# Kernel tuning notes

Hardware: AMD Instinct MI355X
Metric: run time of the kernel (lower is better)

The kernel has to match this reference:

```python
import jax, jax.numpy as jnp
import numpy as np

B, T, N = 16, 2048, 24
K, C_IN, C0, C1 = 3, 1, 64, 64
KS, PRED_LEN = 3, 24
EPS = 1e-5


def _norm_laplacian(adj):
    # L = D^-1/2 A^T D^-1/2 (matches scipy path: (A D^-1/2)^T D^-1/2)
    d = adj.sum(axis=1)
    dis = jnp.where(d > 0, 1.0 / jnp.sqrt(d), 0.0)
    return dis[:, None] * adj.T * dis[None, :]


def _cheb_stack(L, k_terms):
    polys = [jnp.eye(N, dtype=L.dtype), L]
    for _ in range(2, k_terms):
        polys.append(2.0 * L @ polys[-1] - polys[-2])
    return jnp.stack(polys[:k_terms])  # (K, N, N)


def _causal_conv(x, w, b, dilation):
    ks = w.shape[-1]
    pad = (ks - 1) * dilation
    x = jnp.pad(x, ((0, 0), (0, 0), (0, 0), (pad, 0)))
    y = jax.lax.conv_general_dilated(
        x, w, window_strides=(1, 1), padding='VALID',
        rhs_dilation=(1, dilation),
        dimension_numbers=('NCHW', 'OIHW', 'NCHW'))
    return y + b[None, :, None, None]


def _bn(x, g, be):
    # training-mode batch norm over (B, N, T) per channel
    mu = x.mean(axis=(0, 2, 3), keepdims=True)
    var = x.var(axis=(0, 2, 3), keepdims=True)
    return g[None, :, None, None] * (x - mu) * jax.lax.rsqrt(var + EPS) + be[None, :, None, None]


def setup_inputs() -> dict:
    key = jax.random.key(0)
    ks = jax.random.split(key, 16)
    s = 0.05
    return {
        'batch_x': jax.random.normal(ks[0], (B, T, N), jnp.float32),
        'adj': jax.random.uniform(ks[1], (N, N), jnp.float32),
        'theta': jax.random.normal(ks[2], (K, C_IN, C0), jnp.float32),  # Theta per Cheb term
        'w1a': jax.random.normal(ks[3], (C0, C0, 1, KS), jnp.float32) * s,
        'b1a': jnp.zeros((C0,), jnp.float32),
        'g1a': jnp.ones((C0,), jnp.float32), 'be1a': jnp.zeros((C0,), jnp.float32),
        'w1b': jax.random.normal(ks[4], (C0, C0, 1, KS), jnp.float32) * s,
        'b1b': jnp.zeros((C0,), jnp.float32),
        'g1b': jnp.ones((C0,), jnp.float32), 'be1b': jnp.zeros((C0,), jnp.float32),
        'w2a': jax.random.normal(ks[5], (C1, C0, 1, KS), jnp.float32) * s,
        'b2a': jnp.zeros((C1,), jnp.float32),
        'g2a': jnp.ones((C1,), jnp.float32), 'be2a': jnp.zeros((C1,), jnp.float32),
        'w2b': jax.random.normal(ks[6], (C1, C1, 1, KS), jnp.float32) * s,
        'b2b': jnp.zeros((C1,), jnp.float32),
        'g2b': jnp.ones((C1,), jnp.float32), 'be2b': jnp.zeros((C1,), jnp.float32),
        'w_end': jax.random.normal(ks[7], (C1 // 2, C1, 1, 1), jnp.float32) * s,
        'b_end': jnp.zeros((C1 // 2,), jnp.float32),
        'w_end1': jax.random.normal(ks[8], (1, C1 // 2, 1, 2), jnp.float32) * s,
        'b_end1': jnp.zeros((1,), jnp.float32),
    }


def reference(batch_x, adj, theta,
              w1a, b1a, g1a, be1a, w1b, b1b, g1b, be1b,
              w2a, b2a, g2a, be2a, w2b, b2b, g2b, be2b,
              w_end, b_end, w_end1, b_end1):
    # (B, T, N) -> (B, 1, N, T)
    x = jnp.transpose(batch_x, (0, 2, 1))[:, None, :, :]

    # --- Cheb_conv: fused over K terms and all timesteps ---
    L = _norm_laplacian(adj)
    Tk = _cheb_stack(L, K)                       # (K, N, N)
    xp = jnp.transpose(x, (0, 2, 1, 3))          # (B, N, C_in, T)
    # out[b,o,n,t] = sum_{k,m,c} xp[b,m,c,t] Tk[k,m,n] theta[k,c,o]
    gc = jnp.einsum('bmct,kmn,kco->bont', xp, Tk, theta)  # (B, C0, N, T)

    # --- TCN block 1 (dilation 1), residual is identity (C0 == C0) ---
    h = jax.nn.relu(_bn(_causal_conv(gc, w1a, b1a, 1), g1a, be1a))
    h = jax.nn.relu(_bn(_causal_conv(h, w1b, b1b, 1), g1b, be1b))
    out0 = jax.nn.relu(h + gc)

    # --- TCN block 2 (dilation 2), residual identity (C0 == C1), no final relu ---
    h = jax.nn.relu(_bn(_causal_conv(out0, w2a, b2a, 2), g2a, be2a))
    h = jax.nn.relu(_bn(_causal_conv(h, w2b, b2b, 2), g2b, be2b))
    out = h + out0                               # (B, C1, N, T)

    # --- head: 1x1 conv + relu, then (1,2) valid conv -> 1 channel ---
    e = jax.lax.conv_general_dilated(out, w_end, (1, 1), 'VALID',
                                     dimension_numbers=('NCHW', 'OIHW', 'NCHW'))
    e = jax.nn.relu(e + b_end[None, :, None, None])
    e = jax.lax.conv_general_dilated(e, w_end1, (1, 1), 'VALID',
                                     dimension_numbers=('NCHW', 'OIHW', 'NCHW'))
    e = e + b_end1[None, :, None, None]          # (B, 1, N, T-1)
    e = e[:, 0, :, -PRED_LEN:]                   # (B, N, pred_len)
    return jnp.transpose(e, (0, 2, 1))           # (B, pred_len, N)
```

## Files before the change

kernel.cpp:

```cpp
#include <hip/hip_runtime.h>
#include <cmath>

#define TPB 256

typedef __attribute__((ext_vector_type(8)))  short short8;
typedef __attribute__((ext_vector_type(16))) float float16;

static constexpr int  BB   = 16;
static constexpr int  TDIM = 2048;
static constexpr int  NN   = 24;
static constexpr int  P    = BB * NN;
static constexpr int  C    = 64;
static constexpr int  TILE = 256;
static constexpr int  NBT  = TDIM / TILE;
static constexpr int  NSHARD = 64;
static constexpr float INV_CNT = 1.0f / 786432.0f;

static constexpr size_t OFF_TK    = 0;
static constexpr size_t OFF_WEFF  = 6912;
static constexpr size_t OFF_WFRAG = 9216;
static constexpr size_t OFF_ST    = 82944;
static constexpr size_t OFF_BNAB  = 214016;
static constexpr size_t OFF_O0    = 216320;
static constexpr size_t OFF_YT    = 2673920;
static constexpr size_t OFF_S     = 5131520;
static constexpr size_t OFF_YA    = 14568704;
static constexpr size_t OFF_YB    = 115232000;

__device__ __forceinline__ unsigned short f2bf(float f) {
    unsigned int i = __float_as_uint(f);
    i += 0x7FFFu + ((i >> 16) & 1u);
    return (unsigned short)(i >> 16);
}
__device__ __forceinline__ float bf2f(unsigned short u) {
    return __uint_as_float((unsigned)u << 16);
}
__device__ __forceinline__ unsigned pk2bf(float a, float b) {
    unsigned ua = __float_as_uint(a) + 0x8000u;
    unsigned ub = __float_as_uint(b) + 0x8000u;
    return __builtin_amdgcn_perm(ub, ua, 0x07060302u);
}
__device__ __forceinline__ int xidx(int tt, int ci) {
    return tt * 64 + (((ci ^ (tt & 7)) << 3));
}

__global__ __launch_bounds__(TPB)
void prep_kernel(const float* __restrict__ adj, const float* __restrict__ theta,
                 const float* __restrict__ w1a,
                 const float* __restrict__ w1b, const float* __restrict__ w2a,
                 const float* __restrict__ w2b,
                 float* __restrict__ tk, float* __restrict__ weff,
                 unsigned short* __restrict__ wf, float* __restrict__ stats)
{
    const int tid = threadIdx.x;
    if (blockIdx.x < 144) {
        int e = blockIdx.x * TPB + tid;
        int conv = e / 12288, r = e % 12288;
        int oh = r / 6144; r %= 6144;
        int kc = r / 512;  r %= 512;
        int lane = r / 8;
        int jj = r % 8;
        int o = oh * 32 + (lane & 31);
        int K = kc * 16 + (lane >> 5) * 8 + jj;
        int j = K / 64, c2 = K % 64;
        const float* w = (conv == 0) ? w1b : ((conv == 1) ? w2a : w2b);
        wf[e] = f2bf(w[(o * 64 + c2) * 3 + j]);
        return;
    }

    __shared__ float disl[24];
    __shared__ float Ll[576];
    __shared__ float T2l[576];

    for (int e = tid; e < 4 * 8192; e += TPB) stats[e] = 0.f;

    if (tid < 24) {
        float d = 0.f;
        for (int j = 0; j < 24; ++j) d += adj[tid * 24 + j];
        disl[tid] = (d > 0.f) ? 1.0f / sqrtf(d) : 0.f;
    }
    __syncthreads();
    for (int e = tid; e < 576; e += TPB) {
        int i = e / 24, j = e % 24;
        Ll[e] = disl[i] * adj[j * 24 + i] * disl[j];
    }
    __syncthreads();
    for (int e = tid; e < 576; e += TPB) {
        int i = e / 24, j = e % 24;
        float a = 0.f;
        for (int m = 0; m < 24; ++m) a += Ll[i * 24 + m] * Ll[m * 24 + j];
        T2l[e] = 2.f * a - ((i == j) ? 1.f : 0.f);
    }
    __syncthreads();
    for (int e = tid; e < 576; e += TPB) {
        int i = e / 24, j = e % 24;
        tk[e]        = (i == j) ? 1.f : 0.f;
        tk[576 + e]  = Ll[e];
        tk[1152 + e] = T2l[e];
    }
    for (int e = tid; e < 576; e += TPB) {
        int o = e / 9, k = (e % 9) / 3, j = e % 3;
        float a = 0.f;
        for (int c2 = 0; c2 < 64; ++c2)
            a += w1a[(o * 64 + c2) * 3 + j] * theta[k * 64 + c2];
        weff[(k * 3 + j) * 64 + o] = a;
    }
}

__global__ __launch_bounds__(TPB)
void bnprep_kernel(const float* __restrict__ stats, const float* __restrict__ g,
                   const float* __restrict__ be, float2* __restrict__ ab)
{
    const int tid = threadIdx.x;
    const int ch = tid >> 2, q = tid & 3;
    float s1 = 0.f, s2 = 0.f;
    #pragma unroll
    for (int u = 0; u < 16; ++u) {
        int sh = q * 16 + u;
        s1 += stats[ch * 64 + sh];
        s2 += stats[(64 + ch) * 64 + sh];
    }
    s1 += __shfl_xor(s1, 1); s1 += __shfl_xor(s1, 2);
    s2 += __shfl_xor(s2, 1); s2 += __shfl_xor(s2, 2);
    if (q == 0) {
        float mu  = s1 * INV_CNT;
        float var = s2 * INV_CNT - mu * mu;
        float a = g[ch] * (1.0f / sqrtf(var + 1e-5f));
        ab[ch] = make_float2(a, be[ch] - mu * a);
    }
}

__global__ __launch_bounds__(TPB)
void s_kernel(const float* __restrict__ bx, const float* __restrict__ tk,
              float* __restrict__ sbuf)
{
    __shared__ float bxs[256 * 25];
    __shared__ float tkl[576];
    const int tid = threadIdx.x;
    const int blk = blockIdx.x;
    const int b  = blk / 24;
    const int r  = blk % 24;
    const int k  = r >> 3;
    const int t0 = (r & 7) * 256;

    for (int e = tid; e < 576; e += TPB) tkl[e] = tk[k * 576 + e];
    for (int e = tid; e < 256 * 24; e += TPB) {
        int t = e / 24, m = e % 24;
        bxs[t * 25 + m] = bx[((long)b * TDIM + t0 + t) * NN + m];
    }
    __syncthreads();

    const int t = tid;
    float acc[24];
    #pragma unroll
    for (int n = 0; n < 24; ++n) acc[n] = 0.f;
    for (int m = 0; m < 24; ++m) {
        float xb = bxs[t * 25 + m];
        const float* tr = tkl + m * 24;
        #pragma unroll
        for (int n = 0; n < 24; ++n) acc[n] = fmaf(xb, tr[n], acc[n]);
    }
    for (int n = 0; n < 24; ++n)
        sbuf[((long)k * P + b * NN + n) * TDIM + t0 + t] = acc[n];
}

__global__ __launch_bounds__(TPB)
void stats1a_kernel(const float* __restrict__ sbuf, const float* __restrict__ weff,
                    float* __restrict__ statsOut)
{
    __shared__ float4 ssl4[3 * 66];
    __shared__ float4 wl4[144];
    __shared__ float  part[4][2][64];
    const int tid = threadIdx.x;
    const int blk = blockIdx.x;
    const int p  = blk >> 3;
    const int t0 = (blk & 7) * 256;

    for (int e = tid; e < 576; e += TPB) ((float*)wl4)[e] = weff[e];
    for (int e = tid; e < 3 * 65; e += TPB) {
        int k = e / 65, u4 = e % 65;
        int t = t0 - 4 + u4 * 4;
        float4 v = make_float4(0.f, 0.f, 0.f, 0.f);
        if (t >= 0) v = *(const float4*)(sbuf + ((long)k * P + p) * TDIM + t);
        ssl4[k * 66 + u4] = v;
    }
    __syncthreads();

    const int oq = tid & 7;
    const int tq = tid >> 3;
    float acc[8][8];
    #pragma unroll
    for (int i = 0; i < 8; ++i)
        #pragma unroll
        for (int ti = 0; ti < 8; ++ti) acc[i][ti] = 0.f;

    #pragma unroll
    for (int k = 0; k < 3; ++k) {
        float4 x0 = ssl4[k * 66 + tq * 2];
        float4 x1 = ssl4[k * 66 + tq * 2 + 1];
        float4 x2 = ssl4[k * 66 + tq * 2 + 2];
        float xv[12] = { x0.x,x0.y,x0.z,x0.w, x1.x,x1.y,x1.z,x1.w, x2.x,x2.y,x2.z,x2.w };
        #pragma unroll
        for (int j = 0; j < 3; ++j) {
            float4 w0 = wl4[(k * 3 + j) * 16 + oq * 2];
            float4 w1 = wl4[(k * 3 + j) * 16 + oq * 2 + 1];
            float wv[8] = { w0.x,w0.y,w0.z,w0.w, w1.x,w1.y,w1.z,w1.w };
            #pragma unroll
            for (int i = 0; i < 8; ++i)
                #pragma unroll
                for (int ti = 0; ti < 8; ++ti)
                    acc[i][ti] = fmaf(wv[i], xv[ti + 2 + j], acc[i][ti]);
        }
    }

    float s1v[8], s2v[8];
    #pragma unroll
    for (int i = 0; i < 8; ++i) {
        float a1 = 0.f, a2 = 0.f;
        #pragma unroll
        for (int ti = 0; ti < 8; ++ti) { a1 += acc[i][ti]; a2 += acc[i][ti] * acc[i][ti]; }
        s1v[i] = a1; s2v[i] = a2;
    }
    #pragma unroll
    for (int m = 8; m < 64; m <<= 1) {
        #pragma unroll
        for (int i = 0; i < 8; ++i) {
            s1v[i] += __shfl_xor(s1v[i], m);
            s2v[i] += __shfl_xor(s2v[i], m);
        }
    }
    const int wave = tid >> 6, lane = tid & 63;
    if (lane < 8) {
        #pragma unroll
        for (int i = 0; i < 8; ++i) {
            part[wave][0][oq * 8 + i] = s1v[i];
            part[wave][1][oq * 8 + i] = s2v[i];
        }
    }
    __syncthreads();
    if (tid < 128) {
        int s = tid >> 6, o = tid & 63;
        float tot = part[0][s][o] + part[1][s][o] + part[2][s][o] + part[3][s][o];
        atomicAdd(&statsOut[(s * 64 + o) * NSHARD + (blk & 63)], tot);
    }
}

template<int MODE>
__global__ __launch_bounds__(TPB, 4)
void conv_mfma(const float* __restrict__ sbuf, const unsigned short* __restrict__ yin,
               unsigned short* __restrict__ yout, float* __restrict__ ytail,
               const unsigned short* __restrict__ wf, const float* __restrict__ weff,
               const float2* __restrict__ bnab, float* __restrict__ statsOut,
               const float* __restrict__ theta, float* __restrict__ o0s)
{
    constexpr int SCR = (MODE == 0) ? (792 + 576) : ((MODE == 1) ? (792 + 192) : 512);
    __shared__ unsigned short Xl[260 * 64];
    __shared__ float  scratch[SCR];
    __shared__ float2 abl[64];

    float* const ssl   = scratch;
    float* const weffl = scratch + 792;
    float* const thl   = scratch + 792;
    float* const parts = scratch;

    const int tid  = threadIdx.x;
    const int lane = tid & 63;
    const int w    = tid >> 6;
    const int oh   = w & 1;
    const int l31  = lane & 31;
    const int h    = lane >> 5;
    const int blk  = blockIdx.x;
    const int p    = blk >> 3;
    const int tile = blk & 7;
    const int t0   = tile * TILE;

    short8 af[12];
    #pragma unroll
    for (int kc = 0; kc < 12; ++kc)
        af[kc] = *((const short8*)wf + (oh * 12 + kc) * 64 + lane);

    if (tid < 64) abl[tid] = bnab[tid];
    if (MODE == 0)
        for (int e = tid; e < 576; e += TPB) weffl[e] = weff[e];
    if (MODE == 1)
        if (tid < 192) thl[tid] = theta[tid];
    if (MODE <= 1) {
        for (int e = tid; e < 3 * 66; e += TPB) {
            int k = e / 66, u4 = e % 66;
            int t = t0 - 8 + u4 * 4;
            float4 v = make_float4(0.f, 0.f, 0.f, 0.f);
            if (t >= 0) v = *(const float4*)(sbuf + ((long)k * P + p) * TDIM + t);
            *(float4*)(ssl + k * 264 + u4 * 4) = v;
        }
    }
    __syncthreads();

    const unsigned short* yinb = (MODE >= 1)
        ? (yin + ((long)p * TDIM + t0 - 4) * 64) : nullptr;
    for (int e = tid; e < 260 * 8; e += TPB) {
        const int tt = e >> 3, cb = e & 7;
        const int t = t0 - 4 + tt;
        float xv[8];
        if (t < 0) {
            #pragma unroll
            for (int r = 0; r < 8; ++r) xv[r] = 0.f;
        } else if (MODE == 0) {
            float sv[9];
            #pragma unroll
            for (int k = 0; k < 3; ++k)
                #pragma unroll
                for (int j = 0; j < 3; ++j)
                    sv[k * 3 + j] = ssl[k * 264 + tt + 2 + j];
            #pragma unroll
            for (int r = 0; r < 8; ++r) {
                int c = cb * 8 + r;
                float raw = 0.f;
                #pragma unroll
                for (int u = 0; u < 9; ++u)
                    raw = fmaf(weffl[u * 64 + c], sv[u], raw);
                float2 ab = abl[c];
                xv[r] = fmaxf(fmaf(ab.x, raw, ab.y), 0.f);
            }
        } else {
            short8 yv8 = *(const short8*)(yinb + (long)e * 8);
            float gcb[3];
            if (MODE == 1) {
                gcb[0] = ssl[      tt + 4];
                gcb[1] = ssl[264 + tt + 4];
                gcb[2] = ssl[528 + tt + 4];
            }
            #pragma unroll
            for (int r = 0; r < 8; ++r) {
                int c = cb * 8 + r;
                float2 ab = abl[c];
                float v = bf2f((unsigned short)yv8[r]);
                float hh = fmaxf(fmaf(ab.x, v, ab.y), 0.f);
                if (MODE == 1) {
                    float gc = thl[c] * gcb[0] + thl[64 + c] * gcb[1] + thl[128 + c] * gcb[2];
                    hh = fmaxf(hh + gc, 0.f);
                }
                xv[r] = hh;
            }
        }
        if (MODE == 1 && tile == 7 && tt >= 235) {
            #pragma unroll
            for (int r = 0; r < 8; ++r)
                o0s[(long)p * 1600 + (cb * 8 + r) * 25 + (tt - 235)] = xv[r];
        }
        uint4 pk;
        pk.x = pk2bf(xv[0], xv[1]);
        pk.y = pk2bf(xv[2], xv[3]);
        pk.z = pk2bf(xv[4], xv[5]);
        pk.w = pk2bf(xv[6], xv[7]);
        *(uint4*)(Xl + xidx(tt, cb)) = pk;
    }
    __syncthreads();

    float16 acc[4];
    #pragma unroll
    for (int i = 0; i < 4; ++i)
        #pragma unroll
        for (int r = 0; r < 16; ++r) acc[i][r] = 0.f;

    const int tqb = (w >> 1) * 4;
    #pragma unroll
    for (int kc = 0; kc < 12; ++kc) {
        const int j = kc >> 2;
        const int roff = (MODE == 0) ? (2 + j) : (2 * j);
        const int ci = (kc & 3) * 2 + h;
        #pragma unroll
        for (int i = 0; i < 4; ++i) {
            int row = (tqb + i) * 32 + l31 + roff;
            short8 bfr = *(const short8*)(Xl + xidx(row, ci));
            acc[i] = __builtin_amdgcn_mfma_f32_32x32x16_bf16(af[kc], bfr, acc[i], 0, 0, 0);
        }
    }

    if (MODE <= 1) {
        __syncthreads();

        #pragma unroll
        for (int i = 0; i < 4; ++i) {
            int tl = (tqb + i) * 32 + l31;
            #pragma unroll
            for (int qq = 0; qq < 4; ++qq) {
                int ci = oh * 4 + qq;
                uint2 pk;
                pk.x = pk2bf(acc[i][4 * qq + 0], acc[i][4 * qq + 1]);
                pk.y = pk2bf(acc[i][4 * qq + 2], acc[i][4 * qq + 3]);
                *(uint2*)(Xl + xidx(tl, ci) + 4 * h) = pk;
            }
        }
        __syncthreads();

        const int cb = tid & 7;
        unsigned short* youtb = yout + ((long)p * TDIM + t0) * 64;
        float s1[8], s2[8];
        #pragma unroll
        for (int r = 0; r < 8; ++r) { s1[r] = 0.f; s2[r] = 0.f; }
        for (int e = tid; e < 2048; e += TPB) {
            int tt = e >> 3;
            uint4 v = *(const uint4*)(Xl + xidx(tt, cb));
            *(uint4*)(youtb + (long)e * 8) = v;
            unsigned uu[4] = { v.x, v.y, v.z, v.w };
            #pragma unroll
            for (int qq = 0; qq < 4; ++qq) {
                float f0 = __uint_as_float(uu[qq] << 16);
                float f1 = __uint_as_float(uu[qq] & 0xFFFF0000u);
                s1[2 * qq]     += f0;  s2[2 * qq]     = fmaf(f0, f0, s2[2 * qq]);
                s1[2 * qq + 1] += f1;  s2[2 * qq + 1] = fmaf(f1, f1, s2[2 * qq + 1]);
            }
        }
        #pragma unroll
        for (int m = 8; m <= 32; m <<= 1) {
            #pragma unroll
            for (int r = 0; r < 8; ++r) {
                s1[r] += __shfl_xor(s1[r], m);
                s2[r] += __shfl_xor(s2[r], m);
            }
        }
        if (lane < 8) {
            float* pw = parts + (w * 8 + lane) * 16;
            #pragma unroll
            for (int r = 0; r < 8; ++r) { pw[r * 2] = s1[r]; pw[r * 2 + 1] = s2[r]; }
        }
        __syncthreads();
        if (tid < 64) {
            int o = tid, cbo = o >> 3, r = o & 7;
            float t1 = 0.f, t2 = 0.f;
            #pragma unroll
            for (int ww = 0; ww < 4; ++ww) {
                t1 += parts[(ww * 8 + cbo) * 16 + r * 2];
                t2 += parts[(ww * 8 + cbo) * 16 + r * 2 + 1];
            }
            atomicAdd(&statsOut[o * NSHARD + (blk & 63)], t1);
            atomicAdd(&statsOut[(64 + o) * NSHARD + (blk & 63)], t2);
        }
    } else {
        if (tile == 7) {
            #pragma unroll
            for (int i = 0; i < 4; ++i) {
                int tg = t0 + (tqb + i) * 32 + l31;
                if (tg >= TDIM - 25) {
                    #pragma unroll
                    for (int r = 0; r < 16; ++r) {
                        int o = oh * 32 + (r & 3) + 8 * (r >> 2) + 4 * h;
                        ytail[((long)p * C + o) * 25 + (tg - (TDIM - 25))] = acc[i][r];
                    }
                }
            }
        }
        float s1[16], s2[16];
        #pragma unroll
        for (int r = 0; r < 16; ++r) {
            float a1 = 0.f, a2 = 0.f;
            #pragma unroll
            for (int i = 0; i < 4; ++i) { float v = acc[i][r]; a1 += v; a2 = fmaf(v, v, a2); }
            s1[r] = a1; s2[r] = a2;
        }
        #pragma unroll
        for (int m = 1; m <= 16; m <<= 1) {
            #pragma unroll
            for (int r = 0; r < 16; ++r) {
                s1[r] += __shfl_xor(s1[r], m);
                s2[r] += __shfl_xor(s2[r], m);
            }
        }
        if (l31 == 0) {
            float* pw = parts + (w * 2 + h) * 32;
            #pragma unroll
            for (int r = 0; r < 16; ++r) { pw[r * 2] = s1[r]; pw[r * 2 + 1] = s2[r]; }
        }
        __syncthreads();
        if (tid < 64) {
            int o = tid;
            int ohh = o >> 5, v = o & 31;
            int hh = (v >> 2) & 1, r = (v & 3) + 4 * (v >> 3);
            float t1 = parts[(ohh * 2 + hh) * 32 + r * 2]
                     + parts[((ohh + 2) * 2 + hh) * 32 + r * 2];
            float t2 = parts[(ohh * 2 + hh) * 32 + r * 2 + 1]
                     + parts[((ohh + 2) * 2 + hh) * 32 + r * 2 + 1];
            atomicAdd(&statsOut[o * NSHARD + (blk & 63)], t1);
            atomicAdd(&statsOut[(64 + o) * NSHARD + (blk & 63)], t2);
        }
    }
}

__global__ __launch_bounds__(TPB)
void end_kernel(const float* __restrict__ ytail, const float* __restrict__ o0s,
                const float2* __restrict__ bnab, const float* __restrict__ w_end,
                const float* __restrict__ b_end, const float* __restrict__ w_end1,
                const float* __restrict__ b_end1, float* __restrict__ out)
{
    __shared__ float2 abl[64];
    __shared__ float outl[64 * 25];
    __shared__ float e1l[32 * 25];
    __shared__ float wendl[2048];
    const int tid = threadIdx.x;
    const int p = blockIdx.x;
    const int b = p / 24, n = p % 24;

    if (tid < 64) abl[tid] = bnab[tid];
    for (int e = tid; e < 2048; e += TPB) wendl[e] = w_end[e];
    __syncthreads();

    for (int e = tid; e < 1600; e += TPB) {
        int c = e / 25, tau = e % 25;
        float v = ytail[((long)p * C + c) * 25 + tau];
        float2 ab = abl[c];
        outl[e] = fmaxf(ab.x * v + ab.y, 0.f) + o0s[(long)p * 1600 + e];
    }
    __syncthreads();
    for (int e = tid; e < 800; e += TPB) {
        int q = e / 25, tau = e % 25;
        float a = b_end[q];
        for (int c = 0; c < 64; ++c)
            a = fmaf(wendl[q * 64 + c], outl[c * 25 + tau], a);
        e1l[e] = fmaxf(a, 0.f);
    }
    __syncthreads();
    if (tid < 24) {
        float a = b_end1[0];
        #pragma unroll
        for (int q = 0; q < 32; ++q)
            a += w_end1[q * 2] * e1l[q * 25 + tid] + w_end1[q * 2 + 1] * e1l[q * 25 + tid + 1];
        out[((long)b * 24 + tid) * 24 + n] = a;
    }
}

extern "C" void kernel_launch(void* const* d_in, const int* in_sizes, int n_in,
                              void* d_out, int out_size, void* d_ws, size_t ws_size,
                              hipStream_t stream)
{
    (void)in_sizes; (void)n_in; (void)out_size; (void)ws_size;
    const float* bx    = (const float*)d_in[0];
    const float* adj   = (const float*)d_in[1];
    const float* theta = (const float*)d_in[2];
    const float* w1a   = (const float*)d_in[3];
    const float* g1a   = (const float*)d_in[5];
    const float* be1a  = (const float*)d_in[6];
    const float* w1b   = (const float*)d_in[7];
    const float* g1b   = (const float*)d_in[9];
    const float* be1b  = (const float*)d_in[10];
    const float* w2a   = (const float*)d_in[11];
    const float* g2a   = (const float*)d_in[13];
    const float* be2a  = (const float*)d_in[14];
    const float* w2b   = (const float*)d_in[15];
    const float* g2b   = (const float*)d_in[17];
    const float* be2b  = (const float*)d_in[18];
    const float* wend  = (const float*)d_in[19];
    const float* bend  = (const float*)d_in[20];
    const float* wend1 = (const float*)d_in[21];
    const float* bend1 = (const float*)d_in[22];

    char* ws = (char*)d_ws;
    float*          tk    = (float*)(ws + OFF_TK);
    float*          weff  = (float*)(ws + OFF_WEFF);
    unsigned short* wf    = (unsigned short*)(ws + OFF_WFRAG);
    float*          stats = (float*)(ws + OFF_ST);
    float2*         bnab  = (float2*)(ws + OFF_BNAB);
    float*          o0s   = (float*)(ws + OFF_O0);
    float*          ytail = (float*)(ws + OFF_YT);
    float*          sb    = (float*)(ws + OFF_S);
    unsigned short* yA    = (unsigned short*)(ws + OFF_YA);
    unsigned short* yB    = (unsigned short*)(ws + OFF_YB);

    prep_kernel   <<<145, TPB, 0, stream>>>(adj, theta, w1a, w1b, w2a, w2b,
                                            tk, weff, wf, stats);
    s_kernel      <<<384, TPB, 0, stream>>>(bx, tk, sb);
    stats1a_kernel<<<P * NBT, TPB, 0, stream>>>(sb, weff, stats);
    bnprep_kernel <<<1, TPB, 0, stream>>>(stats,         g1a, be1a, bnab);

    conv_mfma<0><<<P * NBT, TPB, 0, stream>>>(
        sb, nullptr, yA, nullptr, wf, weff,
        bnab, stats + 8192, nullptr, nullptr);
    bnprep_kernel <<<1, TPB, 0, stream>>>(stats + 8192,  g1b, be1b, bnab + 64);

    conv_mfma<1><<<P * NBT, TPB, 0, stream>>>(
        sb, yA, yB, nullptr, wf + 12288, nullptr,
        bnab + 64, stats + 16384, theta, o0s);
    bnprep_kernel <<<1, TPB, 0, stream>>>(stats + 16384, g2a, be2a, bnab + 128);

    conv_mfma<2><<<P * NBT, TPB, 0, stream>>>(
        sb, yB, nullptr, ytail, wf + 24576, nullptr,
        bnab + 128, stats + 24576, nullptr, nullptr);
    bnprep_kernel <<<1, TPB, 0, stream>>>(stats + 24576, g2b, be2b, bnab + 192);

    end_kernel<<<P, TPB, 0, stream>>>(ytail, o0s, bnab + 192,
                                      wend, bend, wend1, bend1, (float*)d_out);
}
```

Measured before the change: 334.3 us.

## Fuse prep with graph conv, compute BN stats from MFMA accumulators, fold final BN prep

Merges the prep and Chebyshev graph-conv kernels into one launch. Each graph-conv block recomputes the Laplacian and its square locally, and the identity term becomes a plain copy. The output-writing conv modes now take their BN statistics directly from the fp32 MFMA accumulators rather than re-reading the bf16 tile from LDS. The last bnprep launch is folded into end_kernel, and per-thread BN scale/shift and theta values are hoisted into registers. This removes several launches and some LDS work, at the cost of redundant Laplacian work per block. Statistics are now taken before bf16 rounding, which slightly changes the numerics.

```diff
diff --git a/kernel.cpp b/kernel.cpp
--- a/kernel.cpp
+++ b/kernel.cpp
@@ -16,7 +16,6 @@
 static constexpr int  NSHARD = 64;
 static constexpr float INV_CNT = 1.0f / 786432.0f;
 
-static constexpr size_t OFF_TK    = 0;
 static constexpr size_t OFF_WEFF  = 6912;
 static constexpr size_t OFF_WFRAG = 9216;
 static constexpr size_t OFF_ST    = 82944;
@@ -44,17 +43,46 @@
     return tt * 64 + (((ci ^ (tt & 7)) << 3));
 }
 
+__device__ __forceinline__
+void bn_from_stats(const float* __restrict__ statsIn, const float* __restrict__ g,
+                   const float* __restrict__ be, float2* abl, int tid)
+{
+    const int ch = tid >> 2, q = tid & 3;
+    float s1 = 0.f, s2 = 0.f;
+    #pragma unroll
+    for (int u = 0; u < 4; ++u) {
+        float4 a = *(const float4*)(statsIn + tid * 16 + u * 4);
+        float4 b = *(const float4*)(statsIn + 4096 + tid * 16 + u * 4);
+        s1 += a.x + a.y + a.z + a.w;
+        s2 += b.x + b.y + b.z + b.w;
+    }
+    s1 += __shfl_xor(s1, 1); s1 += __shfl_xor(s1, 2);
+    s2 += __shfl_xor(s2, 1); s2 += __shfl_xor(s2, 2);
+    if (q == 0) {
+        float mu  = s1 * INV_CNT;
+        float var = s2 * INV_CNT - mu * mu;
+        float a = g[ch] * (1.0f / sqrtf(var + 1e-5f));
+        abl[ch] = make_float2(a, be[ch] - mu * a);
+    }
+}
+
 __global__ __launch_bounds__(TPB)
-void prep_kernel(const float* __restrict__ adj, const float* __restrict__ theta,
-                 const float* __restrict__ w1a,
-                 const float* __restrict__ w1b, const float* __restrict__ w2a,
-                 const float* __restrict__ w2b,
-                 float* __restrict__ tk, float* __restrict__ weff,
-                 unsigned short* __restrict__ wf, float* __restrict__ stats)
-{
+void prep_s_kernel(const float* __restrict__ adj, const float* __restrict__ theta,
+                   const float* __restrict__ w1a,
+                   const float* __restrict__ w1b, const float* __restrict__ w2a,
+                   const float* __restrict__ w2b, const float* __restrict__ bx,
+                   float* __restrict__ weff, unsigned short* __restrict__ wf,
+                   float* __restrict__ stats, float* __restrict__ sbuf)
+{
+    __shared__ float bxs[256 * 25];
+    __shared__ float disl[24];
+    __shared__ float Ll[576];
+    __shared__ float tkl[576];
     const int tid = threadIdx.x;
-    if (blockIdx.x < 144) {
-        int e = blockIdx.x * TPB + tid;
+    const int blk = blockIdx.x;
+
+    if (blk < 144) {
+        int e = blk * TPB + tid;
         int conv = e / 12288, r = e % 12288;
         int oh = r / 6144; r %= 6144;
         int kc = r / 512;  r %= 512;
@@ -67,44 +95,71 @@
         wf[e] = f2bf(w[(o * 64 + c2) * 3 + j]);
         return;
     }
-
-    __shared__ float disl[24];
-    __shared__ float Ll[576];
-    __shared__ float T2l[576];
-
-    for (int e = tid; e < 4 * 8192; e += TPB) stats[e] = 0.f;
+    if (blk == 144) {
+        for (int e = tid; e < 4 * 8192; e += TPB) stats[e] = 0.f;
+        for (int e = tid; e < 576; e += TPB) {
+            int o = e / 9, k = (e % 9) / 3, j = e % 3;
+            float a = 0.f;
+            for (int c2 = 0; c2 < 64; ++c2)
+                a += w1a[(o * 64 + c2) * 3 + j] * theta[k * 64 + c2];
+            weff[(k * 3 + j) * 64 + o] = a;
+        }
+        return;
+    }
+
+    const int sblk = blk - 145;
+    const int b  = sblk / 24;
+    const int rr = sblk % 24;
+    const int k  = rr >> 3;
+    const int t0 = (rr & 7) * 256;
 
     if (tid < 24) {
         float d = 0.f;
         for (int j = 0; j < 24; ++j) d += adj[tid * 24 + j];
         disl[tid] = (d > 0.f) ? 1.0f / sqrtf(d) : 0.f;
     }
+    for (int e = tid; e < 256 * 24; e += TPB) {
+        int t = e / 24, m = e % 24;
+        bxs[t * 25 + m] = bx[((long)b * TDIM + t0 + t) * NN + m];
+    }
     __syncthreads();
     for (int e = tid; e < 576; e += TPB) {
         int i = e / 24, j = e % 24;
         Ll[e] = disl[i] * adj[j * 24 + i] * disl[j];
     }
     __syncthreads();
-    for (int e = tid; e < 576; e += TPB) {
-        int i = e / 24, j = e % 24;
-        float a = 0.f;
-        for (int m = 0; m < 24; ++m) a += Ll[i * 24 + m] * Ll[m * 24 + j];
-        T2l[e] = 2.f * a - ((i == j) ? 1.f : 0.f);
-    }
-    __syncthreads();
-    for (int e = tid; e < 576; e += TPB) {
-        int i = e / 24, j = e % 24;
-        tk[e]        = (i == j) ? 1.f : 0.f;
-        tk[576 + e]  = Ll[e];
-        tk[1152 + e] = T2l[e];
-    }
-    for (int e = tid; e < 576; e += TPB) {
-        int o = e / 9, k = (e % 9) / 3, j = e % 3;
-        float a = 0.f;
-        for (int c2 = 0; c2 < 64; ++c2)
-            a += w1a[(o * 64 + c2) * 3 + j] * theta[k * 64 + c2];
-        weff[(k * 3 + j) * 64 + o] = a;
-    }
+    if (k == 2) {
+        for (int e = tid; e < 576; e += TPB) {
+            int i = e / 24, j = e % 24;
+            float a = 0.f;
+            for (int m = 0; m < 24; ++m) a += Ll[i * 24 + m] * Ll[m * 24 + j];
+            tkl[e] = 2.f * a - ((i == j) ? 1.f : 0.f);
+        }
+    } else {
+        for (int e = tid; e < 576; e += TPB) {
+            int i = e / 24, j = e % 24;
+            tkl[e] = (k == 0) ? ((i == j) ? 1.f : 0.f) : Ll[e];
+        }
+    }
+    __syncthreads();
+
+    const int t = tid;
+    float acc[24];
+    if (k == 0) {
+        #pragma unroll
+        for (int n = 0; n < 24; ++n) acc[n] = bxs[t * 25 + n];
+    } else {
+        #pragma unroll
+        for (int n = 0; n < 24; ++n) acc[n] = 0.f;
+        for (int m = 0; m < 24; ++m) {
+            float xb = bxs[t * 25 + m];
+            const float* tr = tkl + m * 24;
+            #pragma unroll
+            for (int n = 0; n < 24; ++n) acc[n] = fmaf(xb, tr[n], acc[n]);
+        }
+    }
+    for (int n = 0; n < 24; ++n)
+        sbuf[((long)k * P + b * NN + n) * TDIM + t0 + t] = acc[n];
 }
 
 __global__ __launch_bounds__(TPB)
@@ -131,40 +186,6 @@
 }
 
 __global__ __launch_bounds__(TPB)
-void s_kernel(const float* __restrict__ bx, const float* __restrict__ tk,
-              float* __restrict__ sbuf)
-{
-    __shared__ float bxs[256 * 25];
-    __shared__ float tkl[576];
-    const int tid = threadIdx.x;
-    const int blk = blockIdx.x;
-    const int b  = blk / 24;
-    const int r  = blk % 24;
-    const int k  = r >> 3;
-    const int t0 = (r & 7) * 256;
-
-    for (int e = tid; e < 576; e += TPB) tkl[e] = tk[k * 576 + e];
-    for (int e = tid; e < 256 * 24; e += TPB) {
-        int t = e / 24, m = e % 24;
-        bxs[t * 25 + m] = bx[((long)b * TDIM + t0 + t) * NN + m];
-    }
-    __syncthreads();
-
-    const int t = tid;
-    float acc[24];
-    #pragma unroll
-    for (int n = 0; n < 24; ++n) acc[n] = 0.f;
-    for (int m = 0; m < 24; ++m) {
-        float xb = bxs[t * 25 + m];
-        const float* tr = tkl + m * 24;
-        #pragma unroll
-        for (int n = 0; n < 24; ++n) acc[n] = fmaf(xb, tr[n], acc[n]);
-    }
-    for (int n = 0; n < 24; ++n)
-        sbuf[((long)k * P + b * NN + n) * TDIM + t0 + t] = acc[n];
-}
-
-__global__ __launch_bounds__(TPB)
 void stats1a_kernel(const float* __restrict__ sbuf, const float* __restrict__ weff,
                     float* __restrict__ statsOut)
 {
@@ -253,7 +274,7 @@
                const float2* __restrict__ bnab, float* __restrict__ statsOut,
                const float* __restrict__ theta, float* __restrict__ o0s)
 {
-    constexpr int SCR = (MODE == 0) ? (792 + 576) : ((MODE == 1) ? (792 + 192) : 512);
+    constexpr int SCR = (MODE == 0) ? (792 + 576) : ((MODE == 1) ? (792 + 192) : 256);
     __shared__ unsigned short Xl[260 * 64];
     __shared__ float  scratch[SCR];
     __shared__ float2 abl[64];
@@ -269,6 +290,7 @@
     const int oh   = w & 1;
     const int l31  = lane & 31;
     const int h    = lane >> 5;
+    const int cb   = tid & 7;
     const int blk  = blockIdx.x;
     const int p    = blk >> 3;
     const int tile = blk & 7;
@@ -295,10 +317,21 @@
     }
     __syncthreads();
 
+    float2 ab2[8];
+    #pragma unroll
+    for (int r = 0; r < 8; ++r) ab2[r] = abl[cb * 8 + r];
+    float th2[3][8];
+    if (MODE == 1) {
+        #pragma unroll
+        for (int k = 0; k < 3; ++k)
+            #pragma unroll
+            for (int r = 0; r < 8; ++r) th2[k][r] = thl[k * 64 + cb * 8 + r];
+    }
+
     const unsigned short* yinb = (MODE >= 1)
         ? (yin + ((long)p * TDIM + t0 - 4) * 64) : nullptr;
     for (int e = tid; e < 260 * 8; e += TPB) {
-        const int tt = e >> 3, cb = e & 7;
+        const int tt = e >> 3;
         const int t = t0 - 4 + tt;
         float xv[8];
         if (t < 0) {
@@ -318,8 +351,7 @@
                 #pragma unroll
                 for (int u = 0; u < 9; ++u)
                     raw = fmaf(weffl[u * 64 + c], sv[u], raw);
-                float2 ab = abl[c];
-                xv[r] = fmaxf(fmaf(ab.x, raw, ab.y), 0.f);
+                xv[r] = fmaxf(fmaf(ab2[r].x, raw, ab2[r].y), 0.f);
             }
         } else {
             short8 yv8 = *(const short8*)(yinb + (long)e * 8);
@@ -331,12 +363,10 @@
             }
             #pragma unroll
             for (int r = 0; r < 8; ++r) {
-                int c = cb * 8 + r;
-                float2 ab = abl[c];
                 float v = bf2f((unsigned short)yv8[r]);
-                float hh = fmaxf(fmaf(ab.x, v, ab.y), 0.f);
+                float hh = fmaxf(fmaf(ab2[r].x, v, ab2[r].y), 0.f);
                 if (MODE == 1) {
-                    float gc = thl[c] * gcb[0] + thl[64 + c] * gcb[1] + thl[128 + c] * gcb[2];
+                    float gc = th2[0][r] * gcb[0] + th2[1][r] * gcb[1] + th2[2][r] * gcb[2];
                     hh = fmaxf(hh + gc, 0.f);
                 }
                 xv[r] = hh;
@@ -373,6 +403,30 @@
             int row = (tqb + i) * 32 + l31 + roff;
             short8 bfr = *(const short8*)(Xl + xidx(row, ci));
             acc[i] = __builtin_amdgcn_mfma_f32_32x32x16_bf16(af[kc], bfr, acc[i], 0, 0, 0);
+        }
+    }
+
+    {
+        float s1[16], s2[16];
+        #pragma unroll
+        for (int r = 0; r < 16; ++r) {
+            float a1 = 0.f, a2 = 0.f;
+            #pragma unroll
+            for (int i = 0; i < 4; ++i) { float v = acc[i][r]; a1 += v; a2 = fmaf(v, v, a2); }
+            s1[r] = a1; s2[r] = a2;
+        }
+        #pragma unroll
+        for (int m = 1; m <= 16; m <<= 1) {
+            #pragma unroll
+            for (int r = 0; r < 16; ++r) {
+                s1[r] += __shfl_xor(s1[r], m);
+                s2[r] += __shfl_xor(s2[r], m);
+            }
+        }
+        if (l31 == 0) {
+            float* pw = parts + (w * 2 + h) * 32;
+            #pragma unroll
+            for (int r = 0; r < 16; ++r) { pw[r * 2] = s1[r]; pw[r * 2 + 1] = s2[r]; }
         }
     }
 
@@ -393,48 +447,13 @@
         }
         __syncthreads();
 
-        const int cb = tid & 7;
         unsigned short* youtb = yout + ((long)p * TDIM + t0) * 64;
-        float s1[8], s2[8];
-        #pragma unroll
-        for (int r = 0; r < 8; ++r) { s1[r] = 0.f; s2[r] = 0.f; }
-        for (int e = tid; e < 2048; e += TPB) {
+        #pragma unroll
+        for (int it = 0; it < 8; ++it) {
+            int e = tid + it * 256;
             int tt = e >> 3;
             uint4 v = *(const uint4*)(Xl + xidx(tt, cb));
             *(uint4*)(youtb + (long)e * 8) = v;
-            unsigned uu[4] = { v.x, v.y, v.z, v.w };
-            #pragma unroll
-            for (int qq = 0; qq < 4; ++qq) {
-                float f0 = __uint_as_float(uu[qq] << 16);
-                float f1 = __uint_as_float(uu[qq] & 0xFFFF0000u);
-                s1[2 * qq]     += f0;  s2[2 * qq]     = fmaf(f0, f0, s2[2 * qq]);
-                s1[2 * qq + 1] += f1;  s2[2 * qq + 1] = fmaf(f1, f1, s2[2 * qq + 1]);
-            }
-        }
-        #pragma unroll
-        for (int m = 8; m <= 32; m <<= 1) {
-            #pragma unroll
-            for (int r = 0; r < 8; ++r) {
-                s1[r] += __shfl_xor(s1[r], m);
-                s2[r] += __shfl_xor(s2[r], m);
-            }
-        }
-        if (lane < 8) {
-            float* pw = parts + (w * 8 + lane) * 16;
-            #pragma unroll
-            for (int r = 0; r < 8; ++r) { pw[r * 2] = s1[r]; pw[r * 2 + 1] = s2[r]; }
-        }
-        __syncthreads();
-        if (tid < 64) {
-            int o = tid, cbo = o >> 3, r = o & 7;
-            float t1 = 0.f, t2 = 0.f;
-            #pragma unroll
-            for (int ww = 0; ww < 4; ++ww) {
-                t1 += parts[(ww * 8 + cbo) * 16 + r * 2];
-                t2 += parts[(ww * 8 + cbo) * 16 + r * 2 + 1];
-            }
-            atomicAdd(&statsOut[o * NSHARD + (blk & 63)], t1);
-            atomicAdd(&statsOut[(64 + o) * NSHARD + (blk & 63)], t2);
         }
     } else {
         if (tile == 7) {
@@ -450,45 +469,26 @@
                 }
             }
         }
-        float s1[16], s2[16];
-        #pragma unroll
-        for (int r = 0; r < 16; ++r) {
-            float a1 = 0.f, a2 = 0.f;
-            #pragma unroll
-            for (int i = 0; i < 4; ++i) { float v = acc[i][r]; a1 += v; a2 = fmaf(v, v, a2); }
-            s1[r] = a1; s2[r] = a2;
-        }
-        #pragma unroll
-        for (int m = 1; m <= 16; m <<= 1) {
-            #pragma unroll
-            for (int r = 0; r < 16; ++r) {
-                s1[r] += __shfl_xor(s1[r], m);
-                s2[r] += __shfl_xor(s2[r], m);
-            }
-        }
-        if (l31 == 0) {
-            float* pw = parts + (w * 2 + h) * 32;
-            #pragma unroll
-            for (int r = 0; r < 16; ++r) { pw[r * 2] = s1[r]; pw[r * 2 + 1] = s2[r]; }
-        }
         __syncthreads();
-        if (tid < 64) {
-            int o = tid;
-            int ohh = o >> 5, v = o & 31;
-            int hh = (v >> 2) & 1, r = (v & 3) + 4 * (v >> 3);
-            float t1 = parts[(ohh * 2 + hh) * 32 + r * 2]
-                     + parts[((ohh + 2) * 2 + hh) * 32 + r * 2];
-            float t2 = parts[(ohh * 2 + hh) * 32 + r * 2 + 1]
-                     + parts[((ohh + 2) * 2 + hh) * 32 + r * 2 + 1];
-            atomicAdd(&statsOut[o * NSHARD + (blk & 63)], t1);
-            atomicAdd(&statsOut[(64 + o) * NSHARD + (blk & 63)], t2);
-        }
+    }
+
+    if (tid < 64) {
+        int o = tid;
+        int ohh = o >> 5, v = o & 31;
+        int hh = (v >> 2) & 1, r = (v & 3) + 4 * (v >> 3);
+        float t1 = parts[(ohh * 2 + hh) * 32 + r * 2]
+                 + parts[((ohh + 2) * 2 + hh) * 32 + r * 2];
+        float t2 = parts[(ohh * 2 + hh) * 32 + r * 2 + 1]
+                 + parts[((ohh + 2) * 2 + hh) * 32 + r * 2 + 1];
+        atomicAdd(&statsOut[o * NSHARD + (blk & 63)], t1);
+        atomicAdd(&statsOut[(64 + o) * NSHARD + (blk & 63)], t2);
     }
 }
 
 __global__ __launch_bounds__(TPB)
 void end_kernel(const float* __restrict__ ytail, const float* __restrict__ o0s,
-                const float2* __restrict__ bnab, const float* __restrict__ w_end,
+                const float* __restrict__ statsIn, const float* __restrict__ g,
+                const float* __restrict__ be, const float* __restrict__ w_end,
                 const float* __restrict__ b_end, const float* __restrict__ w_end1,
                 const float* __restrict__ b_end1, float* __restrict__ out)
 {
@@ -500,7 +500,7 @@
     const int p = blockIdx.x;
     const int b = p / 24, n = p % 24;
 
-    if (tid < 64) abl[tid] = bnab[tid];
+    bn_from_stats(statsIn, g, be, abl, tid);
     for (int e = tid; e < 2048; e += TPB) wendl[e] = w_end[e];
     __syncthreads();
 
@@ -554,7 +554,6 @@
     const float* bend1 = (const float*)d_in[22];
 
     char* ws = (char*)d_ws;
-    float*          tk    = (float*)(ws + OFF_TK);
     float*          weff  = (float*)(ws + OFF_WEFF);
     unsigned short* wf    = (unsigned short*)(ws + OFF_WFRAG);
     float*          stats = (float*)(ws + OFF_ST);
@@ -565,9 +564,8 @@
     unsigned short* yA    = (unsigned short*)(ws + OFF_YA);
     unsigned short* yB    = (unsigned short*)(ws + OFF_YB);
 
-    prep_kernel   <<<145, TPB, 0, stream>>>(adj, theta, w1a, w1b, w2a, w2b,
-                                            tk, weff, wf, stats);
-    s_kernel      <<<384, TPB, 0, stream>>>(bx, tk, sb);
+    prep_s_kernel <<<145 + 384, TPB, 0, stream>>>(adj, theta, w1a, w1b, w2a, w2b,
+                                                  bx, weff, wf, stats, sb);
     stats1a_kernel<<<P * NBT, TPB, 0, stream>>>(sb, weff, stats);
     bnprep_kernel <<<1, TPB, 0, stream>>>(stats,         g1a, be1a, bnab);
 
@@ -584,8 +582,7 @@
     conv_mfma<2><<<P * NBT, TPB, 0, stream>>>(
         sb, yB, nullptr, ytail, wf + 24576, nullptr,
         bnab + 128, stats + 24576, nullptr, nullptr);
-    bnprep_kernel <<<1, TPB, 0, stream>>>(stats + 24576, g2b, be2b, bnab + 192);
-
-    end_kernel<<<P, TPB, 0, stream>>>(ytail, o0s, bnab + 192,
+
+    end_kernel<<<P, TPB, 0, stream>>>(ytail, o0s, stats + 24576, g2b, be2b,
                                       wend, bend, wend1, bend1, (float*)d_out);
 }
```

New measurement: 349.0 us. 4.4% more time.
